# Kernel optimization log

Hardware: AMD Instinct MI355X
Metric: run time of the kernel (lower is better)

## Reference

```python
import jax, jax.numpy as jnp
import numpy as np

DT = 0.001
ALPHA = 20.0  # surrogate-gradient slope (superspike)
V_TH = 1.0

@jax.custom_vjp
def superspike(x):
    return (x > 0).astype(x.dtype)

def _ss_fwd(x):
    return (x > 0).astype(x.dtype), x

def _ss_bwd(x, g):
    return (g / (ALPHA * jnp.abs(x) + 1.0) ** 2,)

superspike.defvjp(_ss_fwd, _ss_bwd)

def setup_inputs() -> dict:
    key = jax.random.key(0)
    k1, k2, k3 = jax.random.split(key, 3)
    B, T, H = 64, 2000, 256
    x = jax.random.normal(k1, (B, T, H), dtype=jnp.float32)
    scale = 1.0 / np.sqrt(H)
    w_in = jax.random.normal(k2, (H, H), dtype=jnp.float32) * scale
    w_rec = jax.random.normal(k3, (H, H), dtype=jnp.float32) * scale
    tau_syn = jnp.full((1, H), 0.1, dtype=jnp.float32)   # tau_syn_inv param
    tau_mem = jnp.full((1, H), 0.05, dtype=jnp.float32)  # tau_mem_inv param
    return {"x": x, "w_in": w_in, "w_rec": w_rec, "tau_syn": tau_syn, "tau_mem": tau_mem}

def reference(x, w_in, w_rec, tau_syn, tau_mem):
    # x: [B, T, H] -> time-major scan, as in the torch forward's permute(1,0,2)
    B, T, H = x.shape
    tau_syn_inv = jnp.clip(tau_syn, 0.0, 1.0)  # (1, H)
    tau_mem_inv = jnp.clip(tau_mem, 0.0, 1.0)  # (1, H)
    xt = jnp.transpose(x, (1, 0, 2))  # [T, B, H]

    z0 = jnp.zeros((B, H), x.dtype)
    v0 = jnp.zeros((B, H), x.dtype)
    i0 = jnp.zeros((B, H), x.dtype)

    def step(carry, x_t):
        z, v, i = carry
        # norse lif_step with v_leak = v_reset = 0
        v_dec = v + DT * tau_mem_inv * (-v + i)
        i_dec = i - DT * tau_syn_inv * i
        z_new = superspike(v_dec - V_TH)
        v_new = (1.0 - z_new) * v_dec
        i_new = i_dec + x_t @ w_in.T + z @ w_rec.T
        return (z_new, v_new, i_new), z_new

    (z_f, v_f, i_f), out = jax.lax.scan(step, (z0, v0, i0), xt)
    return out, z_f, v_f, i_f  # out: [T, B, H] stacked spikes; final LIF state
```

## Files before the change

kernel.cpp:

```cpp
#include <hip/hip_runtime.h>

#define TT 2000
#define BB 64
#define HH 256
#define BH (BB*HH)
#define CH 8
#define NCH (TT/CH)
#define CROWS 128

__device__ __forceinline__ float clip01(float x) { return fminf(fmaxf(x, 0.0f), 1.0f); }

__global__ void transpose2(const float* __restrict__ w_in, const float* __restrict__ w_rec,
                           float* __restrict__ w_inT, float* __restrict__ w_recT) {
    int idx = blockIdx.x * 256 + threadIdx.x;
    int k = idx >> 8, h = idx & 255;
    w_inT[idx]  = w_in[h * HH + k];
    w_recT[idx] = w_rec[h * HH + k];
}

#define BM 128
#define BN 128
#define BK 32
__global__ __launch_bounds__(256) void gemm_xw(const float* __restrict__ X,
                                               const float* __restrict__ WT,
                                               float* __restrict__ OutXW) {
    __shared__ __align__(16) float XsT[BK][BM + 4];
    __shared__ __align__(16) float Ws[BK][BN + 4];
    int tid = threadIdx.x;
    int n0 = blockIdx.x * BM;
    int h0 = blockIdx.y * BN;
    int ty = tid >> 4, tx = tid & 15;
    float acc[8][8] = {};

    for (int kc = 0; kc < HH; kc += BK) {
        {
            int r = tid & 127, kseg = (tid >> 7) * 16;
            const float* src = X + (size_t)(n0 + r) * HH + kc + kseg;
#pragma unroll
            for (int q = 0; q < 4; q++) {
                float4 xv = *(const float4*)(src + q * 4);
                XsT[kseg + q * 4 + 0][r] = xv.x;
                XsT[kseg + q * 4 + 1][r] = xv.y;
                XsT[kseg + q * 4 + 2][r] = xv.z;
                XsT[kseg + q * 4 + 3][r] = xv.w;
            }
        }
        {
            int krow = tid >> 3, cs = (tid & 7) * 16;
            const float* src = WT + (size_t)(kc + krow) * HH + h0 + cs;
#pragma unroll
            for (int q = 0; q < 4; q++) {
                float4 wv = *(const float4*)(src + q * 4);
                *(float4*)&Ws[krow][cs + q * 4] = wv;
            }
        }
        __syncthreads();
#pragma unroll 4
        for (int kk = 0; kk < BK; kk++) {
            float4 a0 = *(const float4*)&XsT[kk][ty * 8];
            float4 a1 = *(const float4*)&XsT[kk][ty * 8 + 4];
            float4 b0 = *(const float4*)&Ws[kk][tx * 8];
            float4 b1 = *(const float4*)&Ws[kk][tx * 8 + 4];
            float a[8] = {a0.x, a0.y, a0.z, a0.w, a1.x, a1.y, a1.z, a1.w};
            float bb[8] = {b0.x, b0.y, b0.z, b0.w, b1.x, b1.y, b1.z, b1.w};
#pragma unroll
            for (int r = 0; r < 8; r++)
#pragma unroll
                for (int c = 0; c < 8; c++)
                    acc[r][c] += a[r] * bb[c];
        }
        __syncthreads();
    }
#pragma unroll
    for (int r = 0; r < 8; r++) {
        int n = n0 + ty * 8 + r;
        int b = n / TT;
        int t = n - b * TT;
        float* dst = OutXW + ((size_t)t * BB + b) * HH + h0 + tx * 8;
        float4 s0 = {acc[r][0], acc[r][1], acc[r][2], acc[r][3]};
        float4 s1 = {acc[r][4], acc[r][5], acc[r][6], acc[r][7]};
        *(float4*)dst = s0;
        *(float4*)(dst + 4) = s1;
    }
}


#define STEP()                                                                      \
    do {                                                                            \
        bool z[4];                                                                  \
        _Pragma("unroll")                                                           \
        for (int j = 0; j < 4; j++) {                                               \
            float vd = vv[j] + am[j] * (ii[j] - vv[j]);      \
            float id = ii[j] - bs[j] * ii[j];                  \
            z[j] = (vd - 1.0f) > 0.0f;                                              \
            float zf = z[j] ? 1.0f : 0.0f;                                          \
            vv[j] = z[j] ? 0.0f : vd;                                               \
            ii[j] = (id + cur[j]) + racc[j];                    \
            __builtin_nontemporal_store(zf, &outp[stoff + j * 64]);                 \
            zl[j] = zf;                                                             \
        }                                                                           \
        stoff += BH;                                                                \
        unsigned long long m0 = __ballot(z[0]);                                     \
        unsigned long long m1 = __ballot(z[1]);                                     \
        unsigned long long m2 = __ballot(z[2]);                                     \
        unsigned long long m3 = __ballot(z[3]);                                     \
        racc[0] = 0.0f; racc[1] = 0.0f; racc[2] = 0.0f; racc[3] = 0.0f;             \
        if ((m0 | m1 | m2 | m3) != 0ull) {                                          \
            unsigned long long m;                                                   \
            m = m0;                                                                 \
            while (m) { int bit = __builtin_ctzll(m); m &= m - 1;                   \
                const float* wr = wcache + (size_t)(bit) * HH + lane;               \
                racc[0] += wr[0]; racc[1] += wr[64];                                \
                racc[2] += wr[128]; racc[3] += wr[192]; }                           \
            m = m1;                                                                 \
            while (m) { int bit = __builtin_ctzll(m); m &= m - 1;                   \
                const float* wr = wcache + (size_t)(64 + bit) * HH + lane;          \
                racc[0] += wr[0]; racc[1] += wr[64];                                \
                racc[2] += wr[128]; racc[3] += wr[192]; }                           \
            m = m2;                                                                 \
            while (m) { int bit = __builtin_ctzll(m); m &= m - 1;                   \
                const float* wr = w_recT + (size_t)(128 + bit) * HH + lane;         \
                racc[0] += wr[0]; racc[1] += wr[64];                                \
                racc[2] += wr[128]; racc[3] += wr[192]; }                           \
            m = m3;                                                                 \
            while (m) { int bit = __builtin_ctzll(m); m &= m - 1;                   \
                const float* wr = w_recT + (size_t)(192 + bit) * HH + lane;         \
                racc[0] += wr[0]; racc[1] += wr[64];                                \
                racc[2] += wr[128]; racc[3] += wr[192]; }                           \
        }                                                                           \
    } while (0)

__global__ __launch_bounds__(128) void scan_lif(const float* __restrict__ tau_syn,
                                                const float* __restrict__ tau_mem,
                                                const float* __restrict__ w_recT,
                                                float* __restrict__ outp) {
    const float DT = 0.001f;
    __shared__ __align__(16) float ring[2 * CH * HH];
    __shared__ __align__(16) float wcache[CROWS * HH];
    int b = blockIdx.x;
    int lane = threadIdx.x & 63;
    int wid = threadIdx.x >> 6;

    {
        const float4* src = (const float4*)w_recT;
        float4* dst = (float4*)wcache;
#pragma unroll
        for (int q = 0; q < (CROWS * HH / 4) / 128; ++q)
            dst[q * 128 + threadIdx.x] = src[q * 128 + threadIdx.x];
    }

    if (wid == 1) {
        float4 rb[CH];
#pragma unroll
        for (int r = 0; r < CH; ++r)
            rb[r] = *(const float4*)(outp + ((size_t)r * BB + b) * HH + 4 * lane);
#pragma unroll
        for (int r = 0; r < CH; ++r)
            *(float4*)&ring[r * HH + 4 * lane] = rb[r];
        __syncthreads();
        for (int c = 0; c < NCH; ++c) {
            if (c + 1 < NCH) {
                int t0 = (c + 1) * CH;
                int lb = ((c + 1) & 1) * (CH * HH);
                float4 sb[CH];
#pragma unroll
                for (int r = 0; r < CH; ++r)
                    sb[r] = *(const float4*)(outp + ((size_t)(t0 + r) * BB + b) * HH + 4 * lane);
#pragma unroll
                for (int r = 0; r < CH; ++r)
                    *(float4*)&ring[lb + r * HH + 4 * lane] = sb[r];
            }
            __syncthreads();
        }
        return;
    }

    int off = b * HH + lane;
    float am[4], bs[4];
#pragma unroll
    for (int j = 0; j < 4; j++) {
        am[j] = DT * clip01(tau_mem[lane + 64 * j]);
        bs[j] = DT * clip01(tau_syn[lane + 64 * j]);
    }

    float vv[4] = {0.f, 0.f, 0.f, 0.f};
    float ii[4] = {0.f, 0.f, 0.f, 0.f};
    float racc[4] = {0.f, 0.f, 0.f, 0.f};
    float zl[4] = {0.f, 0.f, 0.f, 0.f};
    float cur[4], nxt[4];
    unsigned stoff = (unsigned)off;

    __syncthreads();

    for (int c = 0; c < NCH; ++c) {
        int lb = (c & 1) * (CH * HH);
#pragma unroll
        for (int j = 0; j < 4; j++)
            cur[j] = ring[lb + lane + 64 * j];
        for (int u = 0; u < CH - 1; ++u) {
#pragma unroll
            for (int j = 0; j < 4; j++)
                nxt[j] = ring[lb + (u + 1) * HH + lane + 64 * j];
            STEP();
#pragma unroll
            for (int j = 0; j < 4; j++)
                cur[j] = nxt[j];
        }
        STEP();
        __syncthreads();
    }

#pragma unroll
    for (int j = 0; j < 4; j++) {
        outp[(size_t)TT * BH + b * HH + lane + 64 * j] = zl[j];
        outp[(size_t)TT * BH + BH + b * HH + lane + 64 * j] = vv[j];
        outp[(size_t)TT * BH + 2 * BH + b * HH + lane + 64 * j] = ii[j];
    }
}

extern "C" void kernel_launch(void* const* d_in, const int* in_sizes, int n_in,
                              void* d_out, int out_size, void* d_ws, size_t ws_size,
                              hipStream_t stream) {
    const float* x       = (const float*)d_in[0];
    const float* w_in    = (const float*)d_in[1];
    const float* w_rec   = (const float*)d_in[2];
    const float* tau_syn = (const float*)d_in[3];
    const float* tau_mem = (const float*)d_in[4];
    float* out = (float*)d_out;

    float* w_inT  = (float*)d_ws;
    float* w_recT = w_inT + HH * HH;

    transpose2<<<256, 256, 0, stream>>>(w_in, w_rec, w_inT, w_recT);

    dim3 ggrid((BB * TT) / BM, HH / BN);
    gemm_xw<<<ggrid, 256, 0, stream>>>(x, w_inT, out);

    scan_lif<<<BB, 128, 0, stream>>>(tau_syn, tau_mem, w_recT, out);
}
```

Before: 499.9 us.

## Prefetch recurrent weight rows one step ahead and offload spike stores to helper wave

The recurrent weight matrix is stored permuted so that each lane reads its four hidden units as one float4. After each step's ballot, the compute wave prefetches the weight rows for up to four spikes in each half, to be used in the next step's recurrent sum. It falls back to the serial ballot loop only when more than four spikes occur in a half. Spike outputs are now sent as ballot bitmasks through shared memory, and the loader wave writes them to global memory one chunk later, which takes stores off the serial critical path. The cost is more registers, extra shared-memory traffic, and a multiply-add over eight prefetched rows on every step even when few spikes occur.

```diff
diff --git a/kernel.cpp b/kernel.cpp
--- a/kernel.cpp
+++ b/kernel.cpp
@@ -11,11 +11,12 @@
 __device__ __forceinline__ float clip01(float x) { return fminf(fmaxf(x, 0.0f), 1.0f); }
 
 __global__ void transpose2(const float* __restrict__ w_in, const float* __restrict__ w_rec,
-                           float* __restrict__ w_inT, float* __restrict__ w_recT) {
+                           float* __restrict__ w_inT, float* __restrict__ w_recP) {
     int idx = blockIdx.x * 256 + threadIdx.x;
-    int k = idx >> 8, h = idx & 255;
-    w_inT[idx]  = w_in[h * HH + k];
-    w_recT[idx] = w_rec[h * HH + k];
+    int h = idx >> 8, s = idx & 255;
+    w_inT[s * HH + h] = w_in[idx];
+    int l = h & 63, j = h >> 6;
+    w_recP[s * HH + 4 * l + j] = w_rec[idx];
 }
 
 #define BM 128
@@ -85,97 +86,100 @@
 }
 
 
-#define STEP()                                                                      \
-    do {                                                                            \
-        bool z[4];                                                                  \
-        _Pragma("unroll")                                                           \
-        for (int j = 0; j < 4; j++) {                                               \
-            float vd = vv[j] + am[j] * (ii[j] - vv[j]);      \
-            float id = ii[j] - bs[j] * ii[j];                  \
-            z[j] = (vd - 1.0f) > 0.0f;                                              \
-            float zf = z[j] ? 1.0f : 0.0f;                                          \
-            vv[j] = z[j] ? 0.0f : vd;                                               \
-            ii[j] = (id + cur[j]) + racc[j];                    \
-            __builtin_nontemporal_store(zf, &outp[stoff + j * 64]);                 \
-            zl[j] = zf;                                                             \
-        }                                                                           \
-        stoff += BH;                                                                \
-        unsigned long long m0 = __ballot(z[0]);                                     \
-        unsigned long long m1 = __ballot(z[1]);                                     \
-        unsigned long long m2 = __ballot(z[2]);                                     \
-        unsigned long long m3 = __ballot(z[3]);                                     \
-        racc[0] = 0.0f; racc[1] = 0.0f; racc[2] = 0.0f; racc[3] = 0.0f;             \
-        if ((m0 | m1 | m2 | m3) != 0ull) {                                          \
-            unsigned long long m;                                                   \
-            m = m0;                                                                 \
-            while (m) { int bit = __builtin_ctzll(m); m &= m - 1;                   \
-                const float* wr = wcache + (size_t)(bit) * HH + lane;               \
-                racc[0] += wr[0]; racc[1] += wr[64];                                \
-                racc[2] += wr[128]; racc[3] += wr[192]; }                           \
-            m = m1;                                                                 \
-            while (m) { int bit = __builtin_ctzll(m); m &= m - 1;                   \
-                const float* wr = wcache + (size_t)(64 + bit) * HH + lane;          \
-                racc[0] += wr[0]; racc[1] += wr[64];                                \
-                racc[2] += wr[128]; racc[3] += wr[192]; }                           \
-            m = m2;                                                                 \
-            while (m) { int bit = __builtin_ctzll(m); m &= m - 1;                   \
-                const float* wr = w_recT + (size_t)(128 + bit) * HH + lane;         \
-                racc[0] += wr[0]; racc[1] += wr[64];                                \
-                racc[2] += wr[128]; racc[3] += wr[192]; }                           \
-            m = m3;                                                                 \
-            while (m) { int bit = __builtin_ctzll(m); m &= m - 1;                   \
-                const float* wr = w_recT + (size_t)(192 + bit) * HH + lane;         \
-                racc[0] += wr[0]; racc[1] += wr[64];                                \
-                racc[2] += wr[128]; racc[3] += wr[192]; }                           \
-        }                                                                           \
-    } while (0)
+#define EX1(A, B, SOUT) do {                                                        \
+    bool _ua = ((A) != 0ull);                                                       \
+    unsigned long long _pk = _ua ? (A) : (B);                                       \
+    int _bit = (int)__builtin_ctzll(_pk | 0x8000000000000000ull);                   \
+    SOUT = (_ua ? 0 : 64) + _bit;                                                   \
+    unsigned long long _pc = _pk & (_pk - 1ull);                                    \
+    A = _ua ? _pc : (A);                                                            \
+    B = _ua ? (B) : _pc;                                                            \
+} while (0)
 
 __global__ __launch_bounds__(128) void scan_lif(const float* __restrict__ tau_syn,
                                                 const float* __restrict__ tau_mem,
-                                                const float* __restrict__ w_recT,
+                                                const float* __restrict__ w_recP,
                                                 float* __restrict__ outp) {
     const float DT = 0.001f;
     __shared__ __align__(16) float ring[2 * CH * HH];
-    __shared__ __align__(16) float wcache[CROWS * HH];
+    __shared__ __align__(16) float wc[CROWS * HH];
+    __shared__ __align__(16) unsigned long long mb[2][CH][4];
     int b = blockIdx.x;
     int lane = threadIdx.x & 63;
     int wid = threadIdx.x >> 6;
 
     {
-        const float4* src = (const float4*)w_recT;
-        float4* dst = (float4*)wcache;
+        const float4* src = (const float4*)w_recP;
+        float4* dst = (float4*)wc;
 #pragma unroll
         for (int q = 0; q < (CROWS * HH / 4) / 128; ++q)
             dst[q * 128 + threadIdx.x] = src[q * 128 + threadIdx.x];
     }
 
     if (wid == 1) {
-        float4 rb[CH];
-#pragma unroll
-        for (int r = 0; r < CH; ++r)
-            rb[r] = *(const float4*)(outp + ((size_t)r * BB + b) * HH + 4 * lane);
-#pragma unroll
-        for (int r = 0; r < CH; ++r)
-            *(float4*)&ring[r * HH + 4 * lane] = rb[r];
+        {
+            float a0[CH], a1[CH], a2[CH], a3[CH];
+#pragma unroll
+            for (int r = 0; r < CH; ++r) {
+                const float* base = outp + ((size_t)r * BB + b) * HH;
+                a0[r] = base[lane]; a1[r] = base[lane + 64];
+                a2[r] = base[lane + 128]; a3[r] = base[lane + 192];
+            }
+#pragma unroll
+            for (int r = 0; r < CH; ++r) {
+                float4 v = {a0[r], a1[r], a2[r], a3[r]};
+                *(float4*)&ring[r * HH + 4 * lane] = v;
+            }
+        }
         __syncthreads();
         for (int c = 0; c < NCH; ++c) {
             if (c + 1 < NCH) {
                 int t0 = (c + 1) * CH;
-                int lb = ((c + 1) & 1) * (CH * HH);
-                float4 sb[CH];
-#pragma unroll
-                for (int r = 0; r < CH; ++r)
-                    sb[r] = *(const float4*)(outp + ((size_t)(t0 + r) * BB + b) * HH + 4 * lane);
-#pragma unroll
-                for (int r = 0; r < CH; ++r)
-                    *(float4*)&ring[lb + r * HH + 4 * lane] = sb[r];
+                int lb2 = ((c + 1) & 1) * (CH * HH);
+                float a0[CH], a1[CH], a2[CH], a3[CH];
+#pragma unroll
+                for (int r = 0; r < CH; ++r) {
+                    const float* base = outp + ((size_t)(t0 + r) * BB + b) * HH;
+                    a0[r] = base[lane]; a1[r] = base[lane + 64];
+                    a2[r] = base[lane + 128]; a3[r] = base[lane + 192];
+                }
+#pragma unroll
+                for (int r = 0; r < CH; ++r) {
+                    float4 v = {a0[r], a1[r], a2[r], a3[r]};
+                    *(float4*)&ring[lb2 + r * HH + 4 * lane] = v;
+                }
+            }
+            if (c > 0) {
+                int cc = c - 1, ms = cc & 1, t0 = cc * CH;
+#pragma unroll
+                for (int u = 0; u < CH; ++u) {
+                    unsigned long long q0 = mb[ms][u][0], q1 = mb[ms][u][1];
+                    unsigned long long q2 = mb[ms][u][2], q3 = mb[ms][u][3];
+                    float* dst = outp + ((size_t)(t0 + u) * BB + b) * HH + lane;
+                    __builtin_nontemporal_store(((q0 >> lane) & 1) ? 1.0f : 0.0f, dst);
+                    __builtin_nontemporal_store(((q1 >> lane) & 1) ? 1.0f : 0.0f, dst + 64);
+                    __builtin_nontemporal_store(((q2 >> lane) & 1) ? 1.0f : 0.0f, dst + 128);
+                    __builtin_nontemporal_store(((q3 >> lane) & 1) ? 1.0f : 0.0f, dst + 192);
+                }
             }
             __syncthreads();
         }
+        {
+            int cc = NCH - 1, ms = cc & 1, t0 = cc * CH;
+#pragma unroll
+            for (int u = 0; u < CH; ++u) {
+                unsigned long long q0 = mb[ms][u][0], q1 = mb[ms][u][1];
+                unsigned long long q2 = mb[ms][u][2], q3 = mb[ms][u][3];
+                float* dst = outp + ((size_t)(t0 + u) * BB + b) * HH + lane;
+                __builtin_nontemporal_store(((q0 >> lane) & 1) ? 1.0f : 0.0f, dst);
+                __builtin_nontemporal_store(((q1 >> lane) & 1) ? 1.0f : 0.0f, dst + 64);
+                __builtin_nontemporal_store(((q2 >> lane) & 1) ? 1.0f : 0.0f, dst + 128);
+                __builtin_nontemporal_store(((q3 >> lane) & 1) ? 1.0f : 0.0f, dst + 192);
+            }
+        }
         return;
     }
 
-    int off = b * HH + lane;
     float am[4], bs[4];
 #pragma unroll
     for (int j = 0; j < 4; j++) {
@@ -185,28 +189,99 @@
 
     float vv[4] = {0.f, 0.f, 0.f, 0.f};
     float ii[4] = {0.f, 0.f, 0.f, 0.f};
-    float racc[4] = {0.f, 0.f, 0.f, 0.f};
     float zl[4] = {0.f, 0.f, 0.f, 0.f};
-    float cur[4], nxt[4];
-    unsigned stoff = (unsigned)off;
+    float4 slL0 = {0,0,0,0}, slL1 = {0,0,0,0}, slL2 = {0,0,0,0}, slL3 = {0,0,0,0};
+    float4 slH0 = {0,0,0,0}, slH1 = {0,0,0,0}, slH2 = {0,0,0,0}, slH3 = {0,0,0,0};
+    float wtL0 = 0.f, wtL1 = 0.f, wtL2 = 0.f, wtL3 = 0.f;
+    float wtH0 = 0.f, wtH1 = 0.f, wtH2 = 0.f, wtH3 = 0.f;
+    unsigned long long pm0 = 0, pm1 = 0, pm2 = 0, pm3 = 0;
+    bool fbp = false;
 
     __syncthreads();
 
     for (int c = 0; c < NCH; ++c) {
         int lb = (c & 1) * (CH * HH);
 #pragma unroll
-        for (int j = 0; j < 4; j++)
-            cur[j] = ring[lb + lane + 64 * j];
-        for (int u = 0; u < CH - 1; ++u) {
-#pragma unroll
-            for (int j = 0; j < 4; j++)
-                nxt[j] = ring[lb + (u + 1) * HH + lane + 64 * j];
-            STEP();
-#pragma unroll
-            for (int j = 0; j < 4; j++)
-                cur[j] = nxt[j];
-        }
-        STEP();
+        for (int u = 0; u < CH; ++u) {
+            float4 cur = *(const float4*)&ring[lb + u * HH + 4 * lane];
+            bool zz[4]; float id[4];
+#pragma unroll
+            for (int j = 0; j < 4; j++) {
+                float vd = vv[j] + am[j] * (ii[j] - vv[j]);
+                id[j] = ii[j] - bs[j] * ii[j];
+                zz[j] = (vd - 1.0f) > 0.0f;
+                float zf = zz[j] ? 1.0f : 0.0f;
+                vv[j] = zz[j] ? 0.0f : vd;
+                zl[j] = zf;
+            }
+            unsigned long long m0 = __ballot(zz[0]);
+            unsigned long long m1 = __ballot(zz[1]);
+            unsigned long long m2 = __ballot(zz[2]);
+            unsigned long long m3 = __ballot(zz[3]);
+            if (lane == 0) {
+                ulonglong2 w01; w01.x = m0; w01.y = m1;
+                ulonglong2 w23; w23.x = m2; w23.y = m3;
+                *(ulonglong2*)&mb[c & 1][u][0] = w01;
+                *(ulonglong2*)&mb[c & 1][u][2] = w23;
+            }
+            float r0, r1, r2, r3;
+            if (fbp) {
+                r0 = 0.f; r1 = 0.f; r2 = 0.f; r3 = 0.f;
+                unsigned long long m;
+                m = pm0; while (m) { int bit = __builtin_ctzll(m); m &= m - 1;
+                    float4 e = *(const float4*)(wc + (bit << 8) + 4 * lane);
+                    r0 += e.x; r1 += e.y; r2 += e.z; r3 += e.w; }
+                m = pm1; while (m) { int bit = __builtin_ctzll(m); m &= m - 1;
+                    float4 e = *(const float4*)(wc + ((64 + bit) << 8) + 4 * lane);
+                    r0 += e.x; r1 += e.y; r2 += e.z; r3 += e.w; }
+                m = pm2; while (m) { int bit = __builtin_ctzll(m); m &= m - 1;
+                    float4 e = *(const float4*)(w_recP + ((size_t)(128 + bit) << 8) + 4 * lane);
+                    r0 += e.x; r1 += e.y; r2 += e.z; r3 += e.w; }
+                m = pm3; while (m) { int bit = __builtin_ctzll(m); m &= m - 1;
+                    float4 e = *(const float4*)(w_recP + ((size_t)(192 + bit) << 8) + 4 * lane);
+                    r0 += e.x; r1 += e.y; r2 += e.z; r3 += e.w; }
+            } else {
+                r0 = 0.f; r1 = 0.f; r2 = 0.f; r3 = 0.f;
+                r0 += wtL0 * slL0.x; r1 += wtL0 * slL0.y; r2 += wtL0 * slL0.z; r3 += wtL0 * slL0.w;
+                r0 += wtL1 * slL1.x; r1 += wtL1 * slL1.y; r2 += wtL1 * slL1.z; r3 += wtL1 * slL1.w;
+                r0 += wtL2 * slL2.x; r1 += wtL2 * slL2.y; r2 += wtL2 * slL2.z; r3 += wtL2 * slL2.w;
+                r0 += wtL3 * slL3.x; r1 += wtL3 * slL3.y; r2 += wtL3 * slL3.z; r3 += wtL3 * slL3.w;
+                r0 += wtH0 * slH0.x; r1 += wtH0 * slH0.y; r2 += wtH0 * slH0.z; r3 += wtH0 * slH0.w;
+                r0 += wtH1 * slH1.x; r1 += wtH1 * slH1.y; r2 += wtH1 * slH1.z; r3 += wtH1 * slH1.w;
+                r0 += wtH2 * slH2.x; r1 += wtH2 * slH2.y; r2 += wtH2 * slH2.z; r3 += wtH2 * slH2.w;
+                r0 += wtH3 * slH3.x; r1 += wtH3 * slH3.y; r2 += wtH3 * slH3.z; r3 += wtH3 * slH3.w;
+            }
+            ii[0] = (id[0] + cur.x) + r0;
+            ii[1] = (id[1] + cur.y) + r1;
+            ii[2] = (id[2] + cur.z) + r2;
+            ii[3] = (id[3] + cur.w) + r3;
+            int cntL = __popcll(m0) + __popcll(m1);
+            int cntH = __popcll(m2) + __popcll(m3);
+            pm0 = m0; pm1 = m1; pm2 = m2; pm3 = m3;
+            fbp = (cntL > 4) || (cntH > 4);
+            wtL0 = (cntL > 0) ? 1.0f : 0.0f; wtL1 = (cntL > 1) ? 1.0f : 0.0f;
+            wtL2 = (cntL > 2) ? 1.0f : 0.0f; wtL3 = (cntL > 3) ? 1.0f : 0.0f;
+            wtH0 = (cntH > 0) ? 1.0f : 0.0f; wtH1 = (cntH > 1) ? 1.0f : 0.0f;
+            wtH2 = (cntH > 2) ? 1.0f : 0.0f; wtH3 = (cntH > 3) ? 1.0f : 0.0f;
+            if (cntL) {
+                unsigned long long a = m0, bq = m1;
+                int s0, s1, s2, s3;
+                EX1(a, bq, s0); EX1(a, bq, s1); EX1(a, bq, s2); EX1(a, bq, s3);
+                slL0 = *(const float4*)(wc + (s0 << 8) + 4 * lane);
+                slL1 = *(const float4*)(wc + (s1 << 8) + 4 * lane);
+                slL2 = *(const float4*)(wc + (s2 << 8) + 4 * lane);
+                slL3 = *(const float4*)(wc + (s3 << 8) + 4 * lane);
+            }
+            if (cntH) {
+                unsigned long long a = m2, bq = m3;
+                int s0, s1, s2, s3;
+                EX1(a, bq, s0); EX1(a, bq, s1); EX1(a, bq, s2); EX1(a, bq, s3);
+                slH0 = *(const float4*)(w_recP + ((size_t)(128 + s0) << 8) + 4 * lane);
+                slH1 = *(const float4*)(w_recP + ((size_t)(128 + s1) << 8) + 4 * lane);
+                slH2 = *(const float4*)(w_recP + ((size_t)(128 + s2) << 8) + 4 * lane);
+                slH3 = *(const float4*)(w_recP + ((size_t)(128 + s3) << 8) + 4 * lane);
+            }
+        }
         __syncthreads();
     }
 
@@ -229,12 +304,12 @@
     float* out = (float*)d_out;
 
     float* w_inT  = (float*)d_ws;
-    float* w_recT = w_inT + HH * HH;
-
-    transpose2<<<256, 256, 0, stream>>>(w_in, w_rec, w_inT, w_recT);
+    float* w_recP = w_inT + HH * HH;
+
+    transpose2<<<256, 256, 0, stream>>>(w_in, w_rec, w_inT, w_recP);
 
     dim3 ggrid((BB * TT) / BM, HH / BN);
     gemm_xw<<<ggrid, 256, 0, stream>>>(x, w_inT, out);
 
-    scan_lif<<<BB, 128, 0, stream>>>(tau_syn, tau_mem, w_recT, out);
+    scan_lif<<<BB, 128, 0, stream>>>(tau_syn, tau_mem, w_recP, out);
 }
```

Result: slower. 759.5 us (+51.9%).

## Interleave recurrent weights for float4 gathers, add branchless sparse-spike path, widen GEMM BK

Applied to the files above, without the earlier changes.

The recurrent weight matrix is now stored so that each lane's four output columns are contiguous, letting the sparse spike accumulation use one float4 load per active row instead of four scalar loads. When each half has at most four spikes, a branchless path extracts up to four indices per half, issues all the loads up front and masks the unused ones, avoiding serial ctz loops. The input GEMM tile depth BK is doubled to cut loop iterations and syncs. The cost is extra masked loads when few spikes fire, and higher shared-memory use in the GEMM, which may lower occupancy.

```diff
diff --git a/kernel.cpp b/kernel.cpp
--- a/kernel.cpp
+++ b/kernel.cpp
@@ -11,16 +11,17 @@
 __device__ __forceinline__ float clip01(float x) { return fminf(fmaxf(x, 0.0f), 1.0f); }
 
 __global__ void transpose2(const float* __restrict__ w_in, const float* __restrict__ w_rec,
-                           float* __restrict__ w_inT, float* __restrict__ w_recT) {
+                           float* __restrict__ w_inT, float* __restrict__ w_recP) {
     int idx = blockIdx.x * 256 + threadIdx.x;
-    int k = idx >> 8, h = idx & 255;
-    w_inT[idx]  = w_in[h * HH + k];
-    w_recT[idx] = w_rec[h * HH + k];
+    int h = idx >> 8, s = idx & 255;
+    w_inT[s * HH + h] = w_in[idx];
+    int l = h & 63, j = h >> 6;
+    w_recP[s * HH + 4 * l + j] = w_rec[idx];
 }
 
 #define BM 128
 #define BN 128
-#define BK 32
+#define BK 64
 __global__ __launch_bounds__(256) void gemm_xw(const float* __restrict__ X,
                                                const float* __restrict__ WT,
                                                float* __restrict__ OutXW) {
@@ -34,10 +35,10 @@
 
     for (int kc = 0; kc < HH; kc += BK) {
         {
-            int r = tid & 127, kseg = (tid >> 7) * 16;
+            int r = tid & 127, kseg = (tid >> 7) * 32;
             const float* src = X + (size_t)(n0 + r) * HH + kc + kseg;
 #pragma unroll
-            for (int q = 0; q < 4; q++) {
+            for (int q = 0; q < 8; q++) {
                 float4 xv = *(const float4*)(src + q * 4);
                 XsT[kseg + q * 4 + 0][r] = xv.x;
                 XsT[kseg + q * 4 + 1][r] = xv.y;
@@ -46,10 +47,10 @@
             }
         }
         {
-            int krow = tid >> 3, cs = (tid & 7) * 16;
+            int krow = tid >> 2, cs = (tid & 3) * 32;
             const float* src = WT + (size_t)(kc + krow) * HH + h0 + cs;
 #pragma unroll
-            for (int q = 0; q < 4; q++) {
+            for (int q = 0; q < 8; q++) {
                 float4 wv = *(const float4*)(src + q * 4);
                 *(float4*)&Ws[krow][cs + q * 4] = wv;
             }
@@ -85,17 +86,27 @@
 }
 
 
+#define EX1(A, B, SOUT) do {                                                        \
+    bool _ua = ((A) != 0ull);                                                       \
+    unsigned long long _pk = _ua ? (A) : (B);                                       \
+    int _bit = (int)__builtin_ctzll(_pk | 0x8000000000000000ull);                   \
+    SOUT = (_ua ? 0 : 64) + _bit;                                                   \
+    unsigned long long _pc = _pk & (_pk - 1ull);                                    \
+    A = _ua ? _pc : (A);                                                            \
+    B = _ua ? (B) : _pc;                                                            \
+} while (0)
+
 #define STEP()                                                                      \
     do {                                                                            \
-        bool z[4];                                                                  \
+        bool z[4]; float id[4];                                                     \
         _Pragma("unroll")                                                           \
         for (int j = 0; j < 4; j++) {                                               \
             float vd = vv[j] + am[j] * (ii[j] - vv[j]);      \
-            float id = ii[j] - bs[j] * ii[j];                  \
+            id[j] = ii[j] - bs[j] * ii[j];                     \
             z[j] = (vd - 1.0f) > 0.0f;                                              \
             float zf = z[j] ? 1.0f : 0.0f;                                          \
             vv[j] = z[j] ? 0.0f : vd;                                               \
-            ii[j] = (id + cur[j]) + racc[j];                    \
+            ii[j] = (id[j] + cur[j]) + racc[j];                 \
             __builtin_nontemporal_store(zf, &outp[stoff + j * 64]);                 \
             zl[j] = zf;                                                             \
         }                                                                           \
@@ -106,44 +117,70 @@
         unsigned long long m3 = __ballot(z[3]);                                     \
         racc[0] = 0.0f; racc[1] = 0.0f; racc[2] = 0.0f; racc[3] = 0.0f;             \
         if ((m0 | m1 | m2 | m3) != 0ull) {                                          \
-            unsigned long long m;                                                   \
-            m = m0;                                                                 \
-            while (m) { int bit = __builtin_ctzll(m); m &= m - 1;                   \
-                const float* wr = wcache + (size_t)(bit) * HH + lane;               \
-                racc[0] += wr[0]; racc[1] += wr[64];                                \
-                racc[2] += wr[128]; racc[3] += wr[192]; }                           \
-            m = m1;                                                                 \
-            while (m) { int bit = __builtin_ctzll(m); m &= m - 1;                   \
-                const float* wr = wcache + (size_t)(64 + bit) * HH + lane;          \
-                racc[0] += wr[0]; racc[1] += wr[64];                                \
-                racc[2] += wr[128]; racc[3] += wr[192]; }                           \
-            m = m2;                                                                 \
-            while (m) { int bit = __builtin_ctzll(m); m &= m - 1;                   \
-                const float* wr = w_recT + (size_t)(128 + bit) * HH + lane;         \
-                racc[0] += wr[0]; racc[1] += wr[64];                                \
-                racc[2] += wr[128]; racc[3] += wr[192]; }                           \
-            m = m3;                                                                 \
-            while (m) { int bit = __builtin_ctzll(m); m &= m - 1;                   \
-                const float* wr = w_recT + (size_t)(192 + bit) * HH + lane;         \
-                racc[0] += wr[0]; racc[1] += wr[64];                                \
-                racc[2] += wr[128]; racc[3] += wr[192]; }                           \
+            int cntL = __popcll(m0) + __popcll(m1);                                 \
+            int cntH = __popcll(m2) + __popcll(m3);                                 \
+            if (cntL <= 4 && cntH <= 4) {                                           \
+                unsigned long long a, bq;                                           \
+                int sH0, sH1, sH2, sH3, sL0, sL1, sL2, sL3;                         \
+                a = m2; bq = m3;                                                    \
+                EX1(a, bq, sH0); EX1(a, bq, sH1); EX1(a, bq, sH2); EX1(a, bq, sH3); \
+                               \
+                float4 eH0 = *(const float4*)(w_recP + ((size_t)(128 + sH0) << 8) + 4 * lane); \
+                float4 eH1 = *(const float4*)(w_recP + ((size_t)(128 + sH1) << 8) + 4 * lane); \
+                float4 eH2 = *(const float4*)(w_recP + ((size_t)(128 + sH2) << 8) + 4 * lane); \
+                float4 eH3 = *(const float4*)(w_recP + ((size_t)(128 + sH3) << 8) + 4 * lane); \
+                a = m0; bq = m1;                                                    \
+                EX1(a, bq, sL0); EX1(a, bq, sL1); EX1(a, bq, sL2); EX1(a, bq, sL3); \
+                float4 eL0 = *(const float4*)(wc + (sL0 << 8) + 4 * lane);          \
+                float4 eL1 = *(const float4*)(wc + (sL1 << 8) + 4 * lane);          \
+                float4 eL2 = *(const float4*)(wc + (sL2 << 8) + 4 * lane);          \
+                float4 eL3 = *(const float4*)(wc + (sL3 << 8) + 4 * lane);          \
+                float wL0 = (cntL > 0) ? 1.0f : 0.0f, wL1 = (cntL > 1) ? 1.0f : 0.0f; \
+                float wL2 = (cntL > 2) ? 1.0f : 0.0f, wL3 = (cntL > 3) ? 1.0f : 0.0f; \
+                float wH0 = (cntH > 0) ? 1.0f : 0.0f, wH1 = (cntH > 1) ? 1.0f : 0.0f; \
+                float wH2 = (cntH > 2) ? 1.0f : 0.0f, wH3 = (cntH > 3) ? 1.0f : 0.0f; \
+                float r0 = 0.f, r1 = 0.f, r2 = 0.f, r3 = 0.f;                       \
+                r0 += wL0 * eL0.x; r1 += wL0 * eL0.y; r2 += wL0 * eL0.z; r3 += wL0 * eL0.w; \
+                r0 += wL1 * eL1.x; r1 += wL1 * eL1.y; r2 += wL1 * eL1.z; r3 += wL1 * eL1.w; \
+                r0 += wL2 * eL2.x; r1 += wL2 * eL2.y; r2 += wL2 * eL2.z; r3 += wL2 * eL2.w; \
+                r0 += wL3 * eL3.x; r1 += wL3 * eL3.y; r2 += wL3 * eL3.z; r3 += wL3 * eL3.w; \
+                r0 += wH0 * eH0.x; r1 += wH0 * eH0.y; r2 += wH0 * eH0.z; r3 += wH0 * eH0.w; \
+                r0 += wH1 * eH1.x; r1 += wH1 * eH1.y; r2 += wH1 * eH1.z; r3 += wH1 * eH1.w; \
+                r0 += wH2 * eH2.x; r1 += wH2 * eH2.y; r2 += wH2 * eH2.z; r3 += wH2 * eH2.w; \
+                r0 += wH3 * eH3.x; r1 += wH3 * eH3.y; r2 += wH3 * eH3.z; r3 += wH3 * eH3.w; \
+                racc[0] = r0; racc[1] = r1; racc[2] = r2; racc[3] = r3;             \
+            } else {                                                                \
+                unsigned long long m;                                               \
+                m = m0; while (m) { int bit = __builtin_ctzll(m); m &= m - 1;       \
+                    float4 e = *(const float4*)(wc + (bit << 8) + 4 * lane);        \
+                    racc[0] += e.x; racc[1] += e.y; racc[2] += e.z; racc[3] += e.w; } \
+                m = m1; while (m) { int bit = __builtin_ctzll(m); m &= m - 1;       \
+                    float4 e = *(const float4*)(wc + ((64 + bit) << 8) + 4 * lane); \
+                    racc[0] += e.x; racc[1] += e.y; racc[2] += e.z; racc[3] += e.w; } \
+                m = m2; while (m) { int bit = __builtin_ctzll(m); m &= m - 1;       \
+                    float4 e = *(const float4*)(w_recP + ((size_t)(128 + bit) << 8) + 4 * lane); \
+                    racc[0] += e.x; racc[1] += e.y; racc[2] += e.z; racc[3] += e.w; } \
+                m = m3; while (m) { int bit = __builtin_ctzll(m); m &= m - 1;       \
+                    float4 e = *(const float4*)(w_recP + ((size_t)(192 + bit) << 8) + 4 * lane); \
+                    racc[0] += e.x; racc[1] += e.y; racc[2] += e.z; racc[3] += e.w; } \
+            }                                                                       \
         }                                                                           \
     } while (0)
 
 __global__ __launch_bounds__(128) void scan_lif(const float* __restrict__ tau_syn,
                                                 const float* __restrict__ tau_mem,
-                                                const float* __restrict__ w_recT,
+                                                const float* __restrict__ w_recP,
                                                 float* __restrict__ outp) {
     const float DT = 0.001f;
     __shared__ __align__(16) float ring[2 * CH * HH];
-    __shared__ __align__(16) float wcache[CROWS * HH];
+    __shared__ __align__(16) float wc[CROWS * HH];
     int b = blockIdx.x;
     int lane = threadIdx.x & 63;
     int wid = threadIdx.x >> 6;
 
     {
-        const float4* src = (const float4*)w_recT;
-        float4* dst = (float4*)wcache;
+        const float4* src = (const float4*)w_recP;
+        float4* dst = (float4*)wc;
 #pragma unroll
         for (int q = 0; q < (CROWS * HH / 4) / 128; ++q)
             dst[q * 128 + threadIdx.x] = src[q * 128 + threadIdx.x];
@@ -229,12 +266,12 @@
     float* out = (float*)d_out;
 
     float* w_inT  = (float*)d_ws;
-    float* w_recT = w_inT + HH * HH;
-
-    transpose2<<<256, 256, 0, stream>>>(w_in, w_rec, w_inT, w_recT);
+    float* w_recP = w_inT + HH * HH;
+
+    transpose2<<<256, 256, 0, stream>>>(w_in, w_rec, w_inT, w_recP);
 
     dim3 ggrid((BB * TT) / BM, HH / BN);
     gemm_xw<<<ggrid, 256, 0, stream>>>(x, w_inT, out);
 
-    scan_lif<<<BB, 128, 0, stream>>>(tau_syn, tau_mem, w_recT, out);
-}
+    scan_lif<<<BB, 128, 0, stream>>>(tau_syn, tau_mem, w_recP, out);
+}
```

Result: slower. 619.6 us (+24.0%).

## Interleave recurrent weight rows for float4 loads and prefetch first spike rows

Applied to the files above, without the earlier changes.

Lays out the transposed recurrent weights so each lane's four output columns are contiguous, letting every spiking row be read with one float4 load from LDS or global memory instead of four scalar loads. It also peels the first two spike indices out of the ballot masks and issues their weight loads early, with global-memory rows for the upper half fetched before the LDS-resident part is processed, so that latency overlaps. This aims to shorten the serial per-timestep recurrent accumulation, at the cost of more branchy bookkeeping and extra registers.

```diff
diff --git a/kernel.cpp b/kernel.cpp
--- a/kernel.cpp
+++ b/kernel.cpp
@@ -11,11 +11,12 @@
 __device__ __forceinline__ float clip01(float x) { return fminf(fmaxf(x, 0.0f), 1.0f); }
 
 __global__ void transpose2(const float* __restrict__ w_in, const float* __restrict__ w_rec,
-                           float* __restrict__ w_inT, float* __restrict__ w_recT) {
+                           float* __restrict__ w_inT, float* __restrict__ w_recP) {
     int idx = blockIdx.x * 256 + threadIdx.x;
-    int k = idx >> 8, h = idx & 255;
-    w_inT[idx]  = w_in[h * HH + k];
-    w_recT[idx] = w_rec[h * HH + k];
+    int h = idx >> 8, s = idx & 255;
+    w_inT[s * HH + h] = w_in[idx];
+    int l = h & 63, j = h >> 6;
+    w_recP[s * HH + 4 * l + j] = w_rec[idx];
 }
 
 #define BM 128
@@ -85,6 +86,16 @@
 }
 
 
+#define EX1(A, B, SOUT) do {                                                        \
+    bool _ua = ((A) != 0ull);                                                       \
+    unsigned long long _pk = _ua ? (A) : (B);                                       \
+    int _bit = (int)__builtin_ctzll(_pk | 0x8000000000000000ull);                   \
+    SOUT = (_ua ? 0 : 64) + _bit;                                                   \
+    unsigned long long _pc = _pk & (_pk - 1ull);                                    \
+    A = _ua ? _pc : (A);                                                            \
+    B = _ua ? (B) : _pc;                                                            \
+} while (0)
+
 #define STEP()                                                                      \
     do {                                                                            \
         bool z[4];                                                                  \
@@ -105,45 +116,63 @@
         unsigned long long m2 = __ballot(z[2]);                                     \
         unsigned long long m3 = __ballot(z[3]);                                     \
         racc[0] = 0.0f; racc[1] = 0.0f; racc[2] = 0.0f; racc[3] = 0.0f;             \
-        if ((m0 | m1 | m2 | m3) != 0ull) {                                          \
-            unsigned long long m;                                                   \
-            m = m0;                                                                 \
-            while (m) { int bit = __builtin_ctzll(m); m &= m - 1;                   \
-                const float* wr = wcache + (size_t)(bit) * HH + lane;               \
-                racc[0] += wr[0]; racc[1] += wr[64];                                \
-                racc[2] += wr[128]; racc[3] += wr[192]; }                           \
-            m = m1;                                                                 \
-            while (m) { int bit = __builtin_ctzll(m); m &= m - 1;                   \
-                const float* wr = wcache + (size_t)(64 + bit) * HH + lane;          \
-                racc[0] += wr[0]; racc[1] += wr[64];                                \
-                racc[2] += wr[128]; racc[3] += wr[192]; }                           \
-            m = m2;                                                                 \
-            while (m) { int bit = __builtin_ctzll(m); m &= m - 1;                   \
-                const float* wr = w_recT + (size_t)(128 + bit) * HH + lane;         \
-                racc[0] += wr[0]; racc[1] += wr[64];                                \
-                racc[2] += wr[128]; racc[3] += wr[192]; }                           \
-            m = m3;                                                                 \
-            while (m) { int bit = __builtin_ctzll(m); m &= m - 1;                   \
-                const float* wr = w_recT + (size_t)(192 + bit) * HH + lane;         \
-                racc[0] += wr[0]; racc[1] += wr[64];                                \
-                racc[2] += wr[128]; racc[3] += wr[192]; }                           \
+        unsigned long long a2 = m2, b3 = m3;                                        \
+        float4 eh0 = {0.f, 0.f, 0.f, 0.f}, eh1 = {0.f, 0.f, 0.f, 0.f};              \
+        float wh1 = 0.0f;                                                           \
+        bool hasH = (m2 | m3) != 0ull;                                              \
+        if (hasH) {                                   \
+            int t0, t1;                                                             \
+            EX1(a2, b3, t0);                                                        \
+            wh1 = ((a2 | b3) != 0ull) ? 1.0f : 0.0f;                                \
+            EX1(a2, b3, t1);                                                        \
+            eh0 = *(const float4*)(w_recP + ((size_t)(128 + t0) << 8) + 4 * lane);  \
+            eh1 = *(const float4*)(w_recP + ((size_t)(128 + t1) << 8) + 4 * lane);  \
+        }                                                                           \
+        if ((m0 | m1) != 0ull) {                  \
+            unsigned long long a0 = m0, b1 = m1;                                    \
+            int s0, s1;                                                             \
+            EX1(a0, b1, s0);                                                        \
+            float wl1 = ((a0 | b1) != 0ull) ? 1.0f : 0.0f;                          \
+            EX1(a0, b1, s1);                                                        \
+            float4 el0 = *(const float4*)(wc + (s0 << 8) + 4 * lane);               \
+            float4 el1 = *(const float4*)(wc + (s1 << 8) + 4 * lane);               \
+            racc[0] += el0.x; racc[1] += el0.y; racc[2] += el0.z; racc[3] += el0.w; \
+            racc[0] += wl1 * el1.x; racc[1] += wl1 * el1.y;                         \
+            racc[2] += wl1 * el1.z; racc[3] += wl1 * el1.w;                         \
+            while (a0) { int bit = __builtin_ctzll(a0); a0 &= a0 - 1;               \
+                float4 e = *(const float4*)(wc + (bit << 8) + 4 * lane);            \
+                racc[0] += e.x; racc[1] += e.y; racc[2] += e.z; racc[3] += e.w; }   \
+            while (b1) { int bit = __builtin_ctzll(b1); b1 &= b1 - 1;               \
+                float4 e = *(const float4*)(wc + ((64 + bit) << 8) + 4 * lane);     \
+                racc[0] += e.x; racc[1] += e.y; racc[2] += e.z; racc[3] += e.w; }   \
+        }                                                                           \
+        if (hasH) {               \
+            racc[0] += eh0.x; racc[1] += eh0.y; racc[2] += eh0.z; racc[3] += eh0.w; \
+            racc[0] += wh1 * eh1.x; racc[1] += wh1 * eh1.y;                         \
+            racc[2] += wh1 * eh1.z; racc[3] += wh1 * eh1.w;                         \
+            while (a2) { int bit = __builtin_ctzll(a2); a2 &= a2 - 1;               \
+                float4 e = *(const float4*)(w_recP + ((size_t)(128 + bit) << 8) + 4 * lane); \
+                racc[0] += e.x; racc[1] += e.y; racc[2] += e.z; racc[3] += e.w; }   \
+            while (b3) { int bit = __builtin_ctzll(b3); b3 &= b3 - 1;               \
+                float4 e = *(const float4*)(w_recP + ((size_t)(192 + bit) << 8) + 4 * lane); \
+                racc[0] += e.x; racc[1] += e.y; racc[2] += e.z; racc[3] += e.w; }   \
         }                                                                           \
     } while (0)
 
 __global__ __launch_bounds__(128) void scan_lif(const float* __restrict__ tau_syn,
                                                 const float* __restrict__ tau_mem,
-                                                const float* __restrict__ w_recT,
+                                                const float* __restrict__ w_recP,
                                                 float* __restrict__ outp) {
     const float DT = 0.001f;
     __shared__ __align__(16) float ring[2 * CH * HH];
-    __shared__ __align__(16) float wcache[CROWS * HH];
+    __shared__ __align__(16) float wc[CROWS * HH];
     int b = blockIdx.x;
     int lane = threadIdx.x & 63;
     int wid = threadIdx.x >> 6;
 
     {
-        const float4* src = (const float4*)w_recT;
-        float4* dst = (float4*)wcache;
+        const float4* src = (const float4*)w_recP;
+        float4* dst = (float4*)wc;
 #pragma unroll
         for (int q = 0; q < (CROWS * HH / 4) / 128; ++q)
             dst[q * 128 + threadIdx.x] = src[q * 128 + threadIdx.x];
@@ -229,12 +258,12 @@
     float* out = (float*)d_out;
 
     float* w_inT  = (float*)d_ws;
-    float* w_recT = w_inT + HH * HH;
-
-    transpose2<<<256, 256, 0, stream>>>(w_in, w_rec, w_inT, w_recT);
+    float* w_recP = w_inT + HH * HH;
+
+    transpose2<<<256, 256, 0, stream>>>(w_in, w_rec, w_inT, w_recP);
 
     dim3 ggrid((BB * TT) / BM, HH / BN);
     gemm_xw<<<ggrid, 256, 0, stream>>>(x, w_inT, out);
 
-    scan_lif<<<BB, 128, 0, stream>>>(tau_syn, tau_mem, w_recT, out);
-}
+    scan_lif<<<BB, 128, 0, stream>>>(tau_syn, tau_mem, w_recP, out);
+}
```

Measured after the change: 693.0 us. +38.6%, slower.
